# Performance work log

Measured on AMD Instinct MI355X. Metric: run time of the kernel, lower is better.

Reference implementation:

```python
import jax, jax.numpy as jnp
import numpy as np

N_NODES = 100000
N_EDGES = 1600000
IN_DIM, HID_DIM, OUT_DIM = 128, 128, 64


def setup_inputs() -> dict:
    key = jax.random.key(0)
    k1, k2, k3, k4 = jax.random.split(key, 4)
    x = jax.random.normal(k1, (N_NODES, IN_DIM), dtype=jnp.float32)
    edge_index = jax.random.randint(k2, (2, N_EDGES), 0, N_NODES, dtype=jnp.int64)
    W1 = jax.random.normal(k3, (IN_DIM, HID_DIM), dtype=jnp.float32) * (1.0 / np.sqrt(IN_DIM))
    b1 = jnp.zeros((HID_DIM,), dtype=jnp.float32)
    W2 = jax.random.normal(k4, (HID_DIM, OUT_DIM), dtype=jnp.float32) * (1.0 / np.sqrt(HID_DIM))
    b2 = jnp.zeros((OUT_DIM,), dtype=jnp.float32)
    return {"x": x, "edge_index": edge_index, "W1": W1, "b1": b1, "W2": W2, "b2": b2}


def _gcn_conv(h, src, dst, norm, W, b, n_nodes):
    # Dense transform first (PyG GCNConv order), then gather-scatter aggregation.
    h = h @ W                                   # [N, out]
    msg = h[src] * norm[:, None]                # [E, out] gather + scale
    out = jax.ops.segment_sum(msg, dst, num_segments=n_nodes)  # scatter-add
    return out + b


def reference(x, edge_index, W1, b1, W2, b2):
    src, dst = edge_index[0], edge_index[1]
    n = x.shape[0]
    # symmetric normalization: deg from in-degree (unit edge weights), no self loops
    deg = jax.ops.segment_sum(jnp.ones_like(src, dtype=x.dtype), dst, num_segments=n)
    deg_inv_sqrt = jnp.where(deg > 0, jax.lax.rsqrt(jnp.maximum(deg, 1.0)), 0.0)
    norm = deg_inv_sqrt[src] * deg_inv_sqrt[dst]  # [E]
    h = jax.nn.relu(_gcn_conv(x, src, dst, norm, W1, b1, n))
    # dropout is identity in eval mode
    out = _gcn_conv(h, src, dst, norm, W2, b2, n)
    return out
```

## Files before the change

### kernel.cpp

```cpp
#include <hip/hip_runtime.h>
#include <stdint.h>

#define NN 100000
#define NE 1600000
#define K_DIM 128

#define BSH 7
#define NBKT ((NN + (1 << BSH) - 1) >> BSH)
#define EPT 32
#define BIN_CHUNK (256 * EPT)
#define CAP 4096
#define PADE 2301000

typedef unsigned int uint32;
typedef unsigned short ushort16;
typedef __attribute__((ext_vector_type(8))) short bf16x8;
typedef __attribute__((ext_vector_type(4))) float f32x4;

__device__ __forceinline__ ushort16 f2bf(float f) {
    uint32 u = __float_as_uint(f);
    u += 0x7fffu + ((u >> 16) & 1u);
    return (ushort16)(u >> 16);
}
__device__ __forceinline__ float bf_lo(uint32 u) { return __uint_as_float(u << 16); }
__device__ __forceinline__ float bf_hi(uint32 u) { return __uint_as_float(u & 0xffff0000u); }

#define ACC8(v) do { \
    a0 += bf_lo((v).x); a1 += bf_hi((v).x); \
    a2 += bf_lo((v).y); a3 += bf_hi((v).y); \
    a4 += bf_lo((v).z); a5 += bf_hi((v).z); \
    a6 += bf_lo((v).w); a7 += bf_hi((v).w); } while (0)

__device__ __forceinline__ bf16x8 ld_frag8(const ushort16* p) {
    uint2 lo = *(const uint2*)p;
    uint2 hi = *(const uint2*)(p + 4);
    union { uint32 u[4]; bf16x8 v; } x;
    x.u[0] = lo.x; x.u[1] = lo.y; x.u[2] = hi.x; x.u[3] = hi.y;
    return x.v;
}


__global__ __launch_bounds__(256) void bin_pass1_kernel(
        const int* __restrict__ ei, int* __restrict__ gcursor,
        uint32* __restrict__ staging) {
    __shared__ int hist[NBKT];
    __shared__ int base[NBKT];
    int tid = threadIdx.x;
    int e0 = blockIdx.x * BIN_CHUNK;

    for (int i = tid; i < NBKT; i += 256) hist[i] = 0;
    __syncthreads();

    #pragma unroll
    for (int k = 0; k < EPT; k++) {
        int e = e0 + k * 256 + tid;
        if (e < NE) {
            int d = ei[NE + e];
            atomicAdd(&hist[d >> BSH], 1);
        }
    }
    __syncthreads();

    for (int i = tid; i < NBKT; i += 256) {
        int c = hist[i];
        base[i] = c ? atomicAdd(&gcursor[i], c) : 0;
        hist[i] = 0;
    }
    __syncthreads();

    #pragma unroll
    for (int k = 0; k < EPT; k++) {
        int e = e0 + k * 256 + tid;
        if (e < NE) {
            int s = ei[e];
            int d = ei[NE + e];
            int b = d >> BSH;
            int off = atomicAdd(&hist[b], 1);
            staging[(size_t)b * CAP + base[b] + off] =
                ((uint32)s << 7) | (uint32)(d & 127);
        }
    }
}

__global__ __launch_bounds__(256) void bucket_finish_kernel(
        const uint32* __restrict__ staging, const int* __restrict__ gcursor,
        int* __restrict__ gedge, int* __restrict__ deg, float* __restrict__ dis,
        int* __restrict__ row_start, int* __restrict__ ssrc) {
    __shared__ uint32 pairs[CAP];
    __shared__ int cnt[1 << BSH];
    __shared__ int sb[1 << BSH];
    __shared__ int cur[1 << BSH];
    __shared__ int pend[1 << BSH];
    __shared__ int bbase;
    int b = blockIdx.x;
    int node0 = b << BSH;
    int tid = threadIdx.x;
    int n_edges = gcursor[b];

    if (tid < (1 << BSH)) cnt[tid] = 0;
    __syncthreads();

    for (int i = tid; i < n_edges; i += 256) {
        uint32 p = staging[(size_t)b * CAP + i];
        pairs[i] = p;
        atomicAdd(&cnt[p & 127u], 1);
    }
    __syncthreads();

    int p = 0;
    if (tid < (1 << BSH)) {
        int node = node0 + tid;
        int c = cnt[tid];
        if (node < NN) {
            deg[node] = c;
            dis[node] = (c > 0) ? rsqrtf((float)c) : 0.0f;
            p = (c + 7) & ~7;
        }
        sb[tid] = p;
    }
    __syncthreads();
    #pragma unroll
    for (int off = 1; off < (1 << BSH); off <<= 1) {
        int t = (tid >= off && tid < (1 << BSH)) ? sb[tid - off] : 0;
        __syncthreads();
        if (tid < (1 << BSH)) sb[tid] += t;
        __syncthreads();
    }
    if (tid == (1 << BSH) - 1) bbase = atomicAdd(gedge, sb[tid]);
    __syncthreads();

    if (tid < (1 << BSH)) {
        int rs = bbase + sb[tid] - p;
        cur[tid] = rs;
        pend[tid] = rs + p;
        int node = node0 + tid;
        if (node < NN) row_start[node] = rs;
    }
    __syncthreads();

    for (int i = tid; i < n_edges; i += 256) {
        uint32 pr = pairs[i];
        int off = atomicAdd(&cur[pr & 127u], 1);
        ssrc[off] = (int)(pr >> 7);
    }
    __syncthreads();

    if (tid < (1 << BSH)) {
        int node = node0 + tid;
        if (node < NN) {
            for (int q = cur[tid]; q < pend[tid]; q++) ssrc[q] = NN;
        }
    }
}

template <int N, bool ABF16, int ZROWB>
__global__ __launch_bounds__(256) void gemm_mfma_kernel(
        const void* __restrict__ Ap, const float* __restrict__ W,
        const float* __restrict__ dis, ushort16* __restrict__ out, int M) {
    constexpr int BM = 64, K = K_DIM;
    constexpr int LDA = 132;
    constexpr int NT = N / 16;
    constexpr int NLOG = (N == 128) ? 7 : 6;

    __shared__ ushort16 As[BM * LDA];
    __shared__ ushort16 Bt[N * LDA];

    int tid = threadIdx.x;
    int row0 = blockIdx.x * BM;

    if constexpr (ZROWB > 0) {
        if (blockIdx.x == 0 && tid < ZROWB / 4)
            ((uint32*)&out[(size_t)NN * N])[tid] = 0u;
    }

    if constexpr (!ABF16) {
        const float* A = (const float*)Ap;
        #pragma unroll
        for (int c = 0; c < 8; c++) {
            int idx = c * 1024 + tid * 4;
            int r = idx >> 7, col = idx & 127;
            int ra = row0 + r;
            float4 v = (ra < M) ? *(const float4*)&A[(size_t)ra * K + col]
                                : make_float4(0.f, 0.f, 0.f, 0.f);
            ushort4 bq;
            bq.x = f2bf(v.x); bq.y = f2bf(v.y); bq.z = f2bf(v.z); bq.w = f2bf(v.w);
            *(ushort4*)&As[r * LDA + col] = bq;
        }
    } else {
        const ushort16* A = (const ushort16*)Ap;
        #pragma unroll
        for (int c = 0; c < 4; c++) {
            int idx = c * 2048 + tid * 8;
            int r = idx >> 7, col = idx & 127;
            int ra = row0 + r;
            uint4 v = make_uint4(0u, 0u, 0u, 0u);
            if (ra < M) v = *(const uint4*)&A[(size_t)ra * K + col];
            *(uint2*)&As[r * LDA + col]     = make_uint2(v.x, v.y);
            *(uint2*)&As[r * LDA + col + 4] = make_uint2(v.z, v.w);
        }
    }
    {
        #pragma unroll
        for (int c = 0; c < (K * N) / 1024; c++) {
            int idx = c * 1024 + tid * 4;
            int k = idx >> NLOG, n = idx & (N - 1);
            float4 v = *(const float4*)&W[idx];
            Bt[(n + 0) * LDA + k] = f2bf(v.x);
            Bt[(n + 1) * LDA + k] = f2bf(v.y);
            Bt[(n + 2) * LDA + k] = f2bf(v.z);
            Bt[(n + 3) * LDA + k] = f2bf(v.w);
        }
    }
    __syncthreads();

    int lane = tid & 63;
    int wv = tid >> 6;
    int m0 = wv * 16;
    int ml = lane & 15;
    int quad = lane >> 4;

    f32x4 acc[NT];
    #pragma unroll
    for (int i = 0; i < NT; i++) acc[i] = (f32x4){0.f, 0.f, 0.f, 0.f};

    #pragma unroll
    for (int ks = 0; ks < 4; ks++) {
        int kof = ks * 32 + quad * 8;
        bf16x8 a = ld_frag8(&As[(m0 + ml) * LDA + kof]);
        #pragma unroll
        for (int nt = 0; nt < NT; nt++) {
            bf16x8 bb = ld_frag8(&Bt[(nt * 16 + ml) * LDA + kof]);
            acc[nt] = __builtin_amdgcn_mfma_f32_16x16x32_bf16(a, bb, acc[nt], 0, 0, 0);
        }
    }

    #pragma unroll
    for (int r = 0; r < 4; r++) {
        int row = row0 + m0 + quad * 4 + r;
        if (row < M) {
            float s = dis[row];
            #pragma unroll
            for (int nt = 0; nt < NT; nt++)
                out[(size_t)row * N + nt * 16 + ml] = f2bf(acc[nt][r] * s);
        }
    }
}

__global__ __launch_bounds__(256) void agg128_kernel(
        const ushort16* __restrict__ g, const int* __restrict__ row_start,
        const int* __restrict__ deg, const int* __restrict__ ssrc,
        const float* __restrict__ dis, const float* __restrict__ bias,
        ushort16* __restrict__ out) {
    int wave = (blockIdx.x * 256 + threadIdx.x) >> 6;
    int lane = threadIdx.x & 63;
    if (wave >= NN) return;

    int beg = row_start[wave];
    int ecount = (deg[wave] + 7) & ~7;
    float sc = dis[wave];

    int fl = lane & 15;
    int q  = lane >> 4;
    int laneoff = fl * 16;

    int idx = ssrc[beg + lane];

    float a0 = 0.f, a1 = 0.f, a2 = 0.f, a3 = 0.f;
    float a4 = 0.f, a5 = 0.f, a6 = 0.f, a7 = 0.f;

    const char* gb = (const char*)g;
    int nb = ((ecount < 64) ? ecount : 64) >> 3;
    int b = 0;
    for (; b + 2 <= nb; b += 2) {
        int s0a = __shfl(idx, b * 8 + q);
        int s1a = __shfl(idx, b * 8 + 4 + q);
        int s0b = __shfl(idx, b * 8 + 8 + q);
        int s1b = __shfl(idx, b * 8 + 12 + q);
        uint4 v0a = *(const uint4*)(gb + (((uint32)s0a << 8) + laneoff));
        uint4 v1a = *(const uint4*)(gb + (((uint32)s1a << 8) + laneoff));
        uint4 v0b = *(const uint4*)(gb + (((uint32)s0b << 8) + laneoff));
        uint4 v1b = *(const uint4*)(gb + (((uint32)s1b << 8) + laneoff));
        ACC8(v0a); ACC8(v1a); ACC8(v0b); ACC8(v1b);
    }
    if (b < nb) {
        int s0 = __shfl(idx, b * 8 + q);
        int s1 = __shfl(idx, b * 8 + 4 + q);
        uint4 v0 = *(const uint4*)(gb + (((uint32)s0 << 8) + laneoff));
        uint4 v1 = *(const uint4*)(gb + (((uint32)s1 << 8) + laneoff));
        ACC8(v0); ACC8(v1);
    }
    for (int e = beg + 64; e < beg + ecount; e += 8) {
        int idx2 = ssrc[e + (lane & 7)];
        int s0 = __shfl(idx2, q);
        int s1 = __shfl(idx2, 4 + q);
        uint4 v0 = *(const uint4*)(gb + (((uint32)s0 << 8) + laneoff));
        uint4 v1 = *(const uint4*)(gb + (((uint32)s1 << 8) + laneoff));
        ACC8(v0); ACC8(v1);
    }

    a0 += __shfl_xor(a0, 16); a1 += __shfl_xor(a1, 16);
    a2 += __shfl_xor(a2, 16); a3 += __shfl_xor(a3, 16);
    a4 += __shfl_xor(a4, 16); a5 += __shfl_xor(a5, 16);
    a6 += __shfl_xor(a6, 16); a7 += __shfl_xor(a7, 16);
    a0 += __shfl_xor(a0, 32); a1 += __shfl_xor(a1, 32);
    a2 += __shfl_xor(a2, 32); a3 += __shfl_xor(a3, 32);
    a4 += __shfl_xor(a4, 32); a5 += __shfl_xor(a5, 32);
    a6 += __shfl_xor(a6, 32); a7 += __shfl_xor(a7, 32);

    if (lane < 16) {
        float4 bA = *(const float4*)&bias[fl * 8];
        float4 bB = *(const float4*)&bias[fl * 8 + 4];
        float o0 = fmaxf(sc * a0 + bA.x, 0.f);
        float o1 = fmaxf(sc * a1 + bA.y, 0.f);
        float o2 = fmaxf(sc * a2 + bA.z, 0.f);
        float o3 = fmaxf(sc * a3 + bA.w, 0.f);
        float o4 = fmaxf(sc * a4 + bB.x, 0.f);
        float o5 = fmaxf(sc * a5 + bB.y, 0.f);
        float o6 = fmaxf(sc * a6 + bB.z, 0.f);
        float o7 = fmaxf(sc * a7 + bB.w, 0.f);
        uint4 pk;
        pk.x = ((uint32)f2bf(o1) << 16) | (uint32)f2bf(o0);
        pk.y = ((uint32)f2bf(o3) << 16) | (uint32)f2bf(o2);
        pk.z = ((uint32)f2bf(o5) << 16) | (uint32)f2bf(o4);
        pk.w = ((uint32)f2bf(o7) << 16) | (uint32)f2bf(o6);
        *(uint4*)&out[(size_t)wave * 128 + fl * 8] = pk;
    }
}

__global__ __launch_bounds__(256) void agg64_kernel(
        const ushort16* __restrict__ g, const int* __restrict__ row_start,
        const int* __restrict__ deg, const int* __restrict__ ssrc,
        const float* __restrict__ dis, const float* __restrict__ bias,
        float* __restrict__ out) {
    int wave = (blockIdx.x * 256 + threadIdx.x) >> 6;
    int lane = threadIdx.x & 63;
    int half = lane >> 5;
    int l2 = lane & 31;
    int node = wave * 2 + half;
    if (node >= NN) return;

    int beg = row_start[node];
    int ecount = (deg[node] + 7) & ~7;
    float sc = dis[node];

    int fl = l2 & 7;
    int q  = l2 >> 3;
    int laneoff = fl * 16;

    int idx = ssrc[beg + l2];

    float a0 = 0.f, a1 = 0.f, a2 = 0.f, a3 = 0.f;
    float a4 = 0.f, a5 = 0.f, a6 = 0.f, a7 = 0.f;

    const char* gb = (const char*)g;
    int nb = ((ecount < 32) ? ecount : 32) >> 3;
    int b = 0;
    for (; b + 2 <= nb; b += 2) {
        int s0a = __shfl(idx, half * 32 + b * 8 + q);
        int s1a = __shfl(idx, half * 32 + b * 8 + 4 + q);
        int s0b = __shfl(idx, half * 32 + b * 8 + 8 + q);
        int s1b = __shfl(idx, half * 32 + b * 8 + 12 + q);
        uint4 v0a = *(const uint4*)(gb + (((uint32)s0a << 7) + laneoff));
        uint4 v1a = *(const uint4*)(gb + (((uint32)s1a << 7) + laneoff));
        uint4 v0b = *(const uint4*)(gb + (((uint32)s0b << 7) + laneoff));
        uint4 v1b = *(const uint4*)(gb + (((uint32)s1b << 7) + laneoff));
        ACC8(v0a); ACC8(v1a); ACC8(v0b); ACC8(v1b);
    }
    if (b < nb) {
        int s0 = __shfl(idx, half * 32 + b * 8 + q);
        int s1 = __shfl(idx, half * 32 + b * 8 + 4 + q);
        uint4 v0 = *(const uint4*)(gb + (((uint32)s0 << 7) + laneoff));
        uint4 v1 = *(const uint4*)(gb + (((uint32)s1 << 7) + laneoff));
        ACC8(v0); ACC8(v1);
    }
    for (int e = beg + 32; e < beg + ecount; e += 8) {
        int idx2 = ssrc[e + (l2 & 7)];
        int s0 = __shfl(idx2, half * 32 + q);
        int s1 = __shfl(idx2, half * 32 + 4 + q);
        uint4 v0 = *(const uint4*)(gb + (((uint32)s0 << 7) + laneoff));
        uint4 v1 = *(const uint4*)(gb + (((uint32)s1 << 7) + laneoff));
        ACC8(v0); ACC8(v1);
    }

    a0 += __shfl_xor(a0, 8);  a1 += __shfl_xor(a1, 8);
    a2 += __shfl_xor(a2, 8);  a3 += __shfl_xor(a3, 8);
    a4 += __shfl_xor(a4, 8);  a5 += __shfl_xor(a5, 8);
    a6 += __shfl_xor(a6, 8);  a7 += __shfl_xor(a7, 8);
    a0 += __shfl_xor(a0, 16); a1 += __shfl_xor(a1, 16);
    a2 += __shfl_xor(a2, 16); a3 += __shfl_xor(a3, 16);
    a4 += __shfl_xor(a4, 16); a5 += __shfl_xor(a5, 16);
    a6 += __shfl_xor(a6, 16); a7 += __shfl_xor(a7, 16);

    if (l2 < 8) {
        float4 bA = *(const float4*)&bias[fl * 8];
        float4 bB = *(const float4*)&bias[fl * 8 + 4];
        float4 oA = make_float4(sc * a0 + bA.x, sc * a1 + bA.y,
                                sc * a2 + bA.z, sc * a3 + bA.w);
        float4 oB = make_float4(sc * a4 + bB.x, sc * a5 + bB.y,
                                sc * a6 + bB.z, sc * a7 + bB.w);
        *(float4*)&out[(size_t)node * 64 + fl * 8]     = oA;
        *(float4*)&out[(size_t)node * 64 + fl * 8 + 4] = oB;
    }
}

extern "C" void kernel_launch(void* const* d_in, const int* in_sizes, int n_in,
                              void* d_out, int out_size, void* d_ws, size_t ws_size,
                              hipStream_t stream) {
    const float* x  = (const float*)d_in[0];
    const int*   ei = (const int*)d_in[1];
    const float* W1 = (const float*)d_in[2];
    const float* b1 = (const float*)d_in[3];
    const float* W2 = (const float*)d_in[4];
    const float* b2 = (const float*)d_in[5];
    float* out = (float*)d_out;

    char* ws = (char*)d_ws;
    size_t off = 0;
    auto alloc = [&](size_t bytes) {
        void* p = ws + off;
        off = (off + bytes + 255) & ~(size_t)255;
        return p;
    };

    int*      deg_i      = (int*)alloc(NN * 4);
    float*    dis        = (float*)alloc(NN * 4);
    int*      row_start  = (int*)alloc(NN * 4);
    int*      gcursor    = (int*)alloc((NBKT + 1) * 4);
    int*      ssrc       = (int*)alloc((size_t)PADE * 4);
    ushort16* g1         = (ushort16*)alloc((size_t)(NN + 1) * 128 * 2);
    ushort16* h          = (ushort16*)alloc((size_t)NN * 128 * 2);
    uint32*   staging    = (uint32*)g1;
    ushort16* g2         = g1;
    int*      gedge      = gcursor + NBKT;

    hipMemsetAsync(gcursor, 0, (NBKT + 1) * 4, stream);

    bin_pass1_kernel<<<(NE + BIN_CHUNK - 1) / BIN_CHUNK, 256, 0, stream>>>(
        ei, gcursor, staging);
    bucket_finish_kernel<<<NBKT, 256, 0, stream>>>(
        staging, gcursor, gedge, deg_i, dis, row_start, ssrc);

    const int GEMM_BLOCKS = (NN + 63) / 64;
    gemm_mfma_kernel<128, false, 256><<<GEMM_BLOCKS, 256, 0, stream>>>(x, W1, dis, g1, NN);

    const int AGG_BLOCKS = (NN + 3) / 4;
    agg128_kernel<<<AGG_BLOCKS, 256, 0, stream>>>(g1, row_start, deg_i, ssrc, dis, b1, h);

    gemm_mfma_kernel<64, true, 128><<<GEMM_BLOCKS, 256, 0, stream>>>(h, W2, dis, g2, NN);

    const int AGG2_BLOCKS = (NN / 2 + 3) / 4;
    agg64_kernel<<<AGG2_BLOCKS, 256, 0, stream>>>(g2, row_start, deg_i, ssrc, dis, b2, out);
}
```

Measured before the change: 281.9 us.

## Fuse edge binning with first GEMM; apply source normalization during aggregation

Merges the edge-binning pass and the layer-1 GEMM into one heterogeneous launch: the first blocks bin edges and the remaining blocks compute x@W1. Because the GEMM now runs before degrees exist, it no longer pre-scales rows by dis. Instead, agg128 gathers dis[src] per edge and applies it with an FMA. Staging moves into the h buffer so it does not collide with g1. This removes one launch and lets binning and GEMM overlap, at the cost of an extra per-edge dis gather and shuffles in aggregation.

```diff
diff --git a/kernel.cpp b/kernel.cpp
--- a/kernel.cpp
+++ b/kernel.cpp
@@ -9,6 +9,7 @@
 #define NBKT ((NN + (1 << BSH) - 1) >> BSH)
 #define EPT 32
 #define BIN_CHUNK (256 * EPT)
+#define BIN_BLOCKS ((NE + BIN_CHUNK - 1) / BIN_CHUNK)
 #define CAP 4096
 #define PADE 2301000
 
@@ -30,6 +31,12 @@
     a2 += bf_lo((v).y); a3 += bf_hi((v).y); \
     a4 += bf_lo((v).z); a5 += bf_hi((v).z); \
     a6 += bf_lo((v).w); a7 += bf_hi((v).w); } while (0)
+
+#define ACC8S(v,d) do { \
+    a0 = fmaf(d, bf_lo((v).x), a0); a1 = fmaf(d, bf_hi((v).x), a1); \
+    a2 = fmaf(d, bf_lo((v).y), a2); a3 = fmaf(d, bf_hi((v).y), a3); \
+    a4 = fmaf(d, bf_lo((v).z), a4); a5 = fmaf(d, bf_hi((v).z), a5); \
+    a6 = fmaf(d, bf_lo((v).w), a6); a7 = fmaf(d, bf_hi((v).w), a7); } while (0)
 
 __device__ __forceinline__ bf16x8 ld_frag8(const ushort16* p) {
     uint2 lo = *(const uint2*)p;
@@ -39,45 +46,113 @@
     return x.v;
 }
 
-
-__global__ __launch_bounds__(256) void bin_pass1_kernel(
+__global__ __launch_bounds__(256) void binxgemm_kernel(
         const int* __restrict__ ei, int* __restrict__ gcursor,
-        uint32* __restrict__ staging) {
-    __shared__ int hist[NBKT];
-    __shared__ int base[NBKT];
+        uint32* __restrict__ staging,
+        const float* __restrict__ x, const float* __restrict__ W1,
+        ushort16* __restrict__ g1, int M) {
+    __shared__ __align__(16) char smem[50688];
     int tid = threadIdx.x;
-    int e0 = blockIdx.x * BIN_CHUNK;
-
-    for (int i = tid; i < NBKT; i += 256) hist[i] = 0;
-    __syncthreads();
-
-    #pragma unroll
-    for (int k = 0; k < EPT; k++) {
-        int e = e0 + k * 256 + tid;
-        if (e < NE) {
-            int d = ei[NE + e];
-            atomicAdd(&hist[d >> BSH], 1);
-        }
-    }
-    __syncthreads();
-
-    for (int i = tid; i < NBKT; i += 256) {
-        int c = hist[i];
-        base[i] = c ? atomicAdd(&gcursor[i], c) : 0;
-        hist[i] = 0;
-    }
-    __syncthreads();
-
-    #pragma unroll
-    for (int k = 0; k < EPT; k++) {
-        int e = e0 + k * 256 + tid;
-        if (e < NE) {
-            int s = ei[e];
-            int d = ei[NE + e];
-            int b = d >> BSH;
-            int off = atomicAdd(&hist[b], 1);
-            staging[(size_t)b * CAP + base[b] + off] =
-                ((uint32)s << 7) | (uint32)(d & 127);
+
+    if (blockIdx.x < BIN_BLOCKS) {
+        int* hist = (int*)smem;
+        int* base = hist + NBKT;
+        int e0 = blockIdx.x * BIN_CHUNK;
+
+        for (int i = tid; i < NBKT; i += 256) hist[i] = 0;
+        __syncthreads();
+
+        #pragma unroll
+        for (int k = 0; k < EPT; k++) {
+            int e = e0 + k * 256 + tid;
+            if (e < NE) {
+                int d = ei[NE + e];
+                atomicAdd(&hist[d >> BSH], 1);
+            }
+        }
+        __syncthreads();
+
+        for (int i = tid; i < NBKT; i += 256) {
+            int c = hist[i];
+            base[i] = c ? atomicAdd(&gcursor[i], c) : 0;
+            hist[i] = 0;
+        }
+        __syncthreads();
+
+        #pragma unroll
+        for (int k = 0; k < EPT; k++) {
+            int e = e0 + k * 256 + tid;
+            if (e < NE) {
+                int s = ei[e];
+                int d = ei[NE + e];
+                int b = d >> BSH;
+                int off = atomicAdd(&hist[b], 1);
+                staging[(size_t)b * CAP + base[b] + off] =
+                    ((uint32)s << 7) | (uint32)(d & 127);
+            }
+        }
+    } else {
+        constexpr int N = 128, BM = 64, K = K_DIM, LDA = 132, NT = N / 16;
+        ushort16* As = (ushort16*)smem;
+        ushort16* Bt = As + BM * LDA;
+        int bid = (int)blockIdx.x - BIN_BLOCKS;
+        int row0 = bid * BM;
+
+        if (bid == 0 && tid < 64)
+            ((uint32*)&g1[(size_t)NN * N])[tid] = 0u;
+
+        #pragma unroll
+        for (int c = 0; c < 8; c++) {
+            int idx = c * 1024 + tid * 4;
+            int r = idx >> 7, col = idx & 127;
+            int ra = row0 + r;
+            float4 v = (ra < M) ? *(const float4*)&x[(size_t)ra * K + col]
+                                : make_float4(0.f, 0.f, 0.f, 0.f);
+            ushort4 bq;
+            bq.x = f2bf(v.x); bq.y = f2bf(v.y); bq.z = f2bf(v.z); bq.w = f2bf(v.w);
+            *(ushort4*)&As[r * LDA + col] = bq;
+        }
+        #pragma unroll
+        for (int c = 0; c < (K * N) / 1024; c++) {
+            int idx = c * 1024 + tid * 4;
+            int k = idx >> 7, n = idx & (N - 1);
+            float4 v = *(const float4*)&W1[idx];
+            Bt[(n + 0) * LDA + k] = f2bf(v.x);
+            Bt[(n + 1) * LDA + k] = f2bf(v.y);
+            Bt[(n + 2) * LDA + k] = f2bf(v.z);
+            Bt[(n + 3) * LDA + k] = f2bf(v.w);
+        }
+        __syncthreads();
+
+        int lane = tid & 63;
+        int wv = tid >> 6;
+        int m0 = wv * 16;
+        int ml = lane & 15;
+        int quad = lane >> 4;
+
+        f32x4 acc[NT];
+        #pragma unroll
+        for (int i = 0; i < NT; i++) acc[i] = (f32x4){0.f, 0.f, 0.f, 0.f};
+
+        #pragma unroll
+        for (int ks = 0; ks < 4; ks++) {
+            int kof = ks * 32 + quad * 8;
+            bf16x8 a = ld_frag8(&As[(m0 + ml) * LDA + kof]);
+            #pragma unroll
+            for (int nt = 0; nt < NT; nt++) {
+                bf16x8 bb = ld_frag8(&Bt[(nt * 16 + ml) * LDA + kof]);
+                acc[nt] = __builtin_amdgcn_mfma_f32_16x16x32_bf16(a, bb, acc[nt], 0, 0, 0);
+            }
+        }
+
+        #pragma unroll
+        for (int r = 0; r < 4; r++) {
+            int row = row0 + m0 + quad * 4 + r;
+            if (row < M) {
+                #pragma unroll
+                for (int nt = 0; nt < NT; nt++)
+                    g1[(size_t)row * N + nt * 16 + ml] = f2bf(acc[nt][r]);
+            }
         }
     }
 }
@@ -115,6 +190,8 @@
             deg[node] = c;
             dis[node] = (c > 0) ? rsqrtf((float)c) : 0.0f;
             p = (c + 7) & ~7;
+        } else if (node == NN) {
+            dis[NN] = 0.0f;
         }
         sb[tid] = p;
     }
@@ -153,9 +230,9 @@
     }
 }
 
-template <int N, bool ABF16, int ZROWB>
+template <int N, int ZROWB>
 __global__ __launch_bounds__(256) void gemm_mfma_kernel(
-        const void* __restrict__ Ap, const float* __restrict__ W,
+        const ushort16* __restrict__ A, const float* __restrict__ W,
         const float* __restrict__ dis, ushort16* __restrict__ out, int M) {
     constexpr int BM = 64, K = K_DIM;
     constexpr int LDA = 132;
@@ -173,31 +250,15 @@
             ((uint32*)&out[(size_t)NN * N])[tid] = 0u;
     }
 
-    if constexpr (!ABF16) {
-        const float* A = (const float*)Ap;
-        #pragma unroll
-        for (int c = 0; c < 8; c++) {
-            int idx = c * 1024 + tid * 4;
-            int r = idx >> 7, col = idx & 127;
-            int ra = row0 + r;
-            float4 v = (ra < M) ? *(const float4*)&A[(size_t)ra * K + col]
-                                : make_float4(0.f, 0.f, 0.f, 0.f);
-            ushort4 bq;
-            bq.x = f2bf(v.x); bq.y = f2bf(v.y); bq.z = f2bf(v.z); bq.w = f2bf(v.w);
-            *(ushort4*)&As[r * LDA + col] = bq;
-        }
-    } else {
-        const ushort16* A = (const ushort16*)Ap;
-        #pragma unroll
-        for (int c = 0; c < 4; c++) {
-            int idx = c * 2048 + tid * 8;
-            int r = idx >> 7, col = idx & 127;
-            int ra = row0 + r;
-            uint4 v = make_uint4(0u, 0u, 0u, 0u);
-            if (ra < M) v = *(const uint4*)&A[(size_t)ra * K + col];
-            *(uint2*)&As[r * LDA + col]     = make_uint2(v.x, v.y);
-            *(uint2*)&As[r * LDA + col + 4] = make_uint2(v.z, v.w);
-        }
+    #pragma unroll
+    for (int c = 0; c < 4; c++) {
+        int idx = c * 2048 + tid * 8;
+        int r = idx >> 7, col = idx & 127;
+        int ra = row0 + r;
+        uint4 v = make_uint4(0u, 0u, 0u, 0u);
+        if (ra < M) v = *(const uint4*)&A[(size_t)ra * K + col];
+        *(uint2*)&As[r * LDA + col]     = make_uint2(v.x, v.y);
+        *(uint2*)&As[r * LDA + col + 4] = make_uint2(v.z, v.w);
     }
     {
         #pragma unroll
@@ -264,6 +325,8 @@
     int laneoff = fl * 16;
 
     int idx = ssrc[beg + lane];
+    uint32 ci = (uint32)idx; if (ci > (uint32)NN) ci = NN;
+    float dsv = dis[ci];
 
     float a0 = 0.f, a1 = 0.f, a2 = 0.f, a3 = 0.f;
     float a4 = 0.f, a5 = 0.f, a6 = 0.f, a7 = 0.f;
@@ -276,26 +339,35 @@
         int s1a = __shfl(idx, b * 8 + 4 + q);
         int s0b = __shfl(idx, b * 8 + 8 + q);
         int s1b = __shfl(idx, b * 8 + 12 + q);
+        float d0a = __shfl(dsv, b * 8 + q);
+        float d1a = __shfl(dsv, b * 8 + 4 + q);
+        float d0b = __shfl(dsv, b * 8 + 8 + q);
+        float d1b = __shfl(dsv, b * 8 + 12 + q);
         uint4 v0a = *(const uint4*)(gb + (((uint32)s0a << 8) + laneoff));
         uint4 v1a = *(const uint4*)(gb + (((uint32)s1a << 8) + laneoff));
         uint4 v0b = *(const uint4*)(gb + (((uint32)s0b << 8) + laneoff));
         uint4 v1b = *(const uint4*)(gb + (((uint32)s1b << 8) + laneoff));
-        ACC8(v0a); ACC8(v1a); ACC8(v0b); ACC8(v1b);
+        ACC8S(v0a, d0a); ACC8S(v1a, d1a); ACC8S(v0b, d0b); ACC8S(v1b, d1b);
     }
     if (b < nb) {
         int s0 = __shfl(idx, b * 8 + q);
         int s1 = __shfl(idx, b * 8 + 4 + q);
+        float d0 = __shfl(dsv, b * 8 + q);
+        float d1 = __shfl(dsv, b * 8 + 4 + q);
         uint4 v0 = *(const uint4*)(gb + (((uint32)s0 << 8) + laneoff));
         uint4 v1 = *(const uint4*)(gb + (((uint32)s1 << 8) + laneoff));
-        ACC8(v0); ACC8(v1);
+        ACC8S(v0, d0); ACC8S(v1, d1);
     }
     for (int e = beg + 64; e < beg + ecount; e += 8) {
         int idx2 = ssrc[e + (lane & 7)];
+        float dsv2 = dis[idx2];
         int s0 = __shfl(idx2, q);
         int s1 = __shfl(idx2, 4 + q);
+        float d0 = __shfl(dsv2, q);
+        float d1 = __shfl(dsv2, 4 + q);
         uint4 v0 = *(const uint4*)(gb + (((uint32)s0 << 8) + laneoff));
         uint4 v1 = *(const uint4*)(gb + (((uint32)s1 << 8) + laneoff));
-        ACC8(v0); ACC8(v1);
+        ACC8S(v0, d0); ACC8S(v1, d1);
     }
 
     a0 += __shfl_xor(a0, 16); a1 += __shfl_xor(a1, 16);
@@ -423,30 +495,30 @@
     };
 
     int*      deg_i      = (int*)alloc(NN * 4);
-    float*    dis        = (float*)alloc(NN * 4);
+    float*    dis        = (float*)alloc((NN + 1) * 4);
     int*      row_start  = (int*)alloc(NN * 4);
     int*      gcursor    = (int*)alloc((NBKT + 1) * 4);
     int*      ssrc       = (int*)alloc((size_t)PADE * 4);
     ushort16* g1         = (ushort16*)alloc((size_t)(NN + 1) * 128 * 2);
-    ushort16* h          = (ushort16*)alloc((size_t)NN * 128 * 2);
-    uint32*   staging    = (uint32*)g1;
+    char*     big        = (char*)alloc((size_t)NN * 128 * 2);
+    uint32*   staging    = (uint32*)big;
+    ushort16* h          = (ushort16*)big;
     ushort16* g2         = g1;
     int*      gedge      = gcursor + NBKT;
 
     hipMemsetAsync(gcursor, 0, (NBKT + 1) * 4, stream);
 
-    bin_pass1_kernel<<<(NE + BIN_CHUNK - 1) / BIN_CHUNK, 256, 0, stream>>>(
-        ei, gcursor, staging);
+    binxgemm_kernel<<<BIN_BLOCKS + (NN + 63) / 64, 256, 0, stream>>>(
+        ei, gcursor, staging, x, W1, g1, NN);
+
     bucket_finish_kernel<<<NBKT, 256, 0, stream>>>(
         staging, gcursor, gedge, deg_i, dis, row_start, ssrc);
 
-    const int GEMM_BLOCKS = (NN + 63) / 64;
-    gemm_mfma_kernel<128, false, 256><<<GEMM_BLOCKS, 256, 0, stream>>>(x, W1, dis, g1, NN);
-
     const int AGG_BLOCKS = (NN + 3) / 4;
     agg128_kernel<<<AGG_BLOCKS, 256, 0, stream>>>(g1, row_start, deg_i, ssrc, dis, b1, h);
 
-    gemm_mfma_kernel<64, true, 128><<<GEMM_BLOCKS, 256, 0, stream>>>(h, W2, dis, g2, NN);
+    const int GEMM_BLOCKS = (NN + 63) / 64;
+    gemm_mfma_kernel<64, 128><<<GEMM_BLOCKS, 256, 0, stream>>>(h, W2, dis, g2, NN);
 
     const int AGG2_BLOCKS = (NN / 2 + 3) / 4;
     agg64_kernel<<<AGG2_BLOCKS, 256, 0, stream>>>(g2, row_start, deg_i, ssrc, dis, b2, out);
```

Result: faster. 265.2 us (-5.9%).
